# Optimization experiments

Measured on AMD Instinct MI355X. Metric: run time of the kernel, lower is better.

Reference implementation:

```python
import jax, jax.numpy as jnp
import numpy as np

H = 50000   # hidden_size
IN = 50000  # in_size
NNZ = 800000
B = 8
T = 32


def spmm(indices, values, num_rows, x):
    """COO sparse @ dense. indices: (2, nnz) int, values: (nnz,), x: (K, N)."""
    rows, cols = indices[0], indices[1]
    contrib = values[:, None] * x[cols]          # (nnz, N) gather + scale
    return jax.ops.segment_sum(contrib, rows, num_segments=num_rows)  # (M, N)


def setup_inputs() -> dict:
    key = jax.random.key(0)
    k1, k2, k3, k4, k5 = jax.random.split(key, 5)
    x = jax.random.normal(k1, (B, T, IN), dtype=jnp.float32)
    hh_indices = jax.random.randint(k2, (2, NNZ), 0, H)
    hh_values = jax.random.normal(k3, (NNZ,), dtype=jnp.float32) * 0.1
    hh_bias = jnp.zeros((H, 1), dtype=jnp.float32)
    ih_indices = jax.random.randint(k4, (2, NNZ), 0, IN)
    ih_values = jax.random.normal(k5, (NNZ,), dtype=jnp.float32) * 0.1
    return {"x": x, "hh_values": hh_values, "hh_bias": hh_bias,
            "ih_values": ih_values, "hh_indices": hh_indices,
            "ih_indices": ih_indices}


def reference(x, hh_values, hh_bias, ih_values, hh_indices, ih_indices):
    # x: (B, T, IN) batch_first -> (T, IN, B) as in _format_x
    xt = jnp.transpose(x, (1, 2, 0))
    h0 = jnp.zeros((H, x.shape[0]), dtype=x.dtype)  # zeros init, (H, B)

    def step(h, x_t):
        pre = (spmm(hh_indices, hh_values, H, h) + hh_bias
               + spmm(ih_indices, ih_values, H, x_t))
        h_new = jnp.tanh(pre)  # layernorm is Identity (use_layernorm=False)
        return h_new, h_new

    _, hs = jax.lax.scan(step, h0, xt)       # (T, H, B)
    return jnp.transpose(hs, (2, 0, 1))      # (B, T, H) batch_first
```

## Files before the change

### kernel.cpp

```cpp
#include <hip/hip_runtime.h>
#include <math.h>

#define HSZ 50000
#define INSZ 50000
#define NNZc 800000
#define BSZ 8
#define TSZ 32

#define CHUNK 2048
#define NBLK ((NNZc + CHUNK - 1) / CHUNK)
#define NCB 196
#define HWORDS (256 * NBLK)
#define NC2 ((HWORDS + 1023) / 1024)

#define NPB 1008
#define GRPS 8
#define GCNT (NPB / GRPS)
#define ROWS_SWEEP (NPB * 32)

typedef _Float16 half8 __attribute__((ext_vector_type(8)));
typedef _Float16 half4 __attribute__((ext_vector_type(4)));

__device__ __forceinline__ unsigned f2h_bits(float f) {
    _Float16 h = (_Float16)f;
    unsigned short u;
    __builtin_memcpy(&u, &h, 2);
    return (unsigned)u;
}
__device__ __forceinline__ float h_bits2f(unsigned u) {
    unsigned short us = (unsigned short)u;
    _Float16 h;
    __builtin_memcpy(&h, &us, 2);
    return (float)h;
}


__global__ void p1_count(const int* __restrict__ hh_idx, const int* __restrict__ ih_idx,
                         int* __restrict__ ghist) {
    const int* rows = blockIdx.y ? ih_idx : hh_idx;
    __shared__ int cnt[256];
    int tid = threadIdx.x;
    cnt[tid] = 0;
    __syncthreads();
    int base = blockIdx.x * CHUNK;
    int nElem = min(CHUNK, NNZc - base);
    for (int k = tid; k < nElem; k += 256) {
        atomicAdd(&cnt[rows[base + k] >> 8], 1);
    }
    __syncthreads();
    ghist[((size_t)blockIdx.y * 256 + tid) * NBLK + blockIdx.x] = cnt[tid];
}

__global__ void p2scanA(int* __restrict__ ghist, int* __restrict__ partials) {
    int* g = ghist + (size_t)blockIdx.y * HWORDS;
    __shared__ int sm[1024];
    int tid = threadIdx.x;
    int idx = blockIdx.x * 1024 + tid;
    int v = (idx < HWORDS) ? g[idx] : 0;
    sm[tid] = v;
    __syncthreads();
    int x = v;
    for (int off = 1; off < 1024; off <<= 1) {
        int y = (tid >= off) ? sm[tid - off] : 0;
        __syncthreads();
        x += y;
        sm[tid] = x;
        __syncthreads();
    }
    if (idx < HWORDS) g[idx] = x - v;
    if (tid == 1023) partials[blockIdx.y * 128 + blockIdx.x] = x;
}

__global__ void p2scanB(int* __restrict__ partials) {
    __shared__ int sm[128];
    int tid = threadIdx.x;
    for (int m = 0; m < 2; ++m) {
        int v = (tid < NC2) ? partials[m * 128 + tid] : 0;
        sm[tid] = v;
        __syncthreads();
        int x = v;
        for (int off = 1; off < 128; off <<= 1) {
            int y = (tid >= off) ? sm[tid - off] : 0;
            __syncthreads();
            x += y;
            sm[tid] = x;
            __syncthreads();
        }
        if (tid < NC2) partials[m * 128 + tid] = x - v;
        __syncthreads();
    }
}

__global__ void p2scanC(int* __restrict__ ghist, const int* __restrict__ partials,
                        int* __restrict__ cbs) {
    int mat = blockIdx.y;
    int* g = ghist + (size_t)mat * HWORDS;
    int i = blockIdx.x * 256 + threadIdx.x;
    if (i < HWORDS) {
        int v = g[i] + partials[mat * 128 + (i >> 10)];
        g[i] = v;
        int b = i / NBLK;
        if (i - b * NBLK == 0 && b < NCB) cbs[mat * (NCB + 1) + b] = v;
    }
    if (i == 0) cbs[mat * (NCB + 1) + NCB] = NNZc;
}

__global__ void p2_part(const int* __restrict__ hh_idx, const float* __restrict__ hh_v,
                        const int* __restrict__ ih_idx, const float* __restrict__ ih_v,
                        const int* __restrict__ ghist,
                        uint2* __restrict__ tmp_hh, uint2* __restrict__ tmp_ih) {
    int mat = blockIdx.y;
    const int* idx = mat ? ih_idx : hh_idx;
    const float* val = mat ? ih_v : hh_v;
    uint2* tmp = mat ? tmp_ih : tmp_hh;
    const int* g = ghist + (size_t)mat * HWORDS;

    __shared__ int cnt[256];
    __shared__ int lstart[256];
    __shared__ int scanbuf[256];
    __shared__ int gbase[256];
    __shared__ uint2 stage[CHUNK];

    int tid = threadIdx.x;
    int base = blockIdx.x * CHUNK;
    int nElem = min(CHUNK, NNZc - base);

    cnt[tid] = 0;
    gbase[tid] = g[(size_t)tid * NBLK + blockIdx.x];
    __syncthreads();
    for (int k = tid; k < nElem; k += 256) {
        atomicAdd(&cnt[idx[base + k] >> 8], 1);
    }
    __syncthreads();
    int v = cnt[tid];
    scanbuf[tid] = v;
    __syncthreads();
    int x = v;
    for (int off = 1; off < 256; off <<= 1) {
        int y = (tid >= off) ? scanbuf[tid - off] : 0;
        __syncthreads();
        x += y;
        scanbuf[tid] = x;
        __syncthreads();
    }
    lstart[tid] = x - v;
    cnt[tid] = 0;
    __syncthreads();
    for (int k = tid; k < nElem; k += 256) {
        int r = idx[base + k];
        int c = idx[NNZc + base + k];
        int b = r >> 8;
        int rank = atomicAdd(&cnt[b], 1);
        stage[lstart[b] + rank] = make_uint2(((unsigned)r << 16) | (unsigned)c,
                                             __float_as_uint(val[base + k]));
    }
    __syncthreads();
    for (int k = tid; k < nElem; k += 256) {
        uint2 el = stage[k];
        int b = el.x >> 24;
        tmp[gbase[b] + (k - lstart[b])] = el;
    }
}

__global__ void p3_final(const int* __restrict__ cbs,
                         const uint2* __restrict__ tmp_hh, const uint2* __restrict__ tmp_ih,
                         int* __restrict__ ptr_hh, int* __restrict__ ptr_ih,
                         unsigned* __restrict__ cv_hh, unsigned* __restrict__ cv_ih) {
    int mat = blockIdx.y;
    const uint2* tmp = mat ? tmp_ih : tmp_hh;
    int* ptr = mat ? ptr_ih : ptr_hh;
    unsigned* cv = mat ? cv_ih : cv_hh;
    __shared__ int rcnt[256];
    __shared__ int rstart[256];
    __shared__ int scanbuf[256];
    int cb = blockIdx.x;
    int row0 = cb << 8;
    int nrows = min(256, HSZ - row0);
    int s = cbs[mat * (NCB + 1) + cb];
    int e = cbs[mat * (NCB + 1) + cb + 1];
    int tid = threadIdx.x;
    rcnt[tid] = 0;
    __syncthreads();
    for (int k = s + tid; k < e; k += 256) {
        atomicAdd(&rcnt[(tmp[k].x >> 16) & 255], 1);
    }
    __syncthreads();
    int v = rcnt[tid];
    scanbuf[tid] = v;
    __syncthreads();
    int x = v;
    for (int off = 1; off < 256; off <<= 1) {
        int y = (tid >= off) ? scanbuf[tid - off] : 0;
        __syncthreads();
        x += y;
        scanbuf[tid] = x;
        __syncthreads();
    }
    rstart[tid] = x - v;
    if (tid < nrows) ptr[row0 + tid] = s + x - v;
    if (cb == NCB - 1 && tid == 0) ptr[HSZ] = NNZc;
    rcnt[tid] = 0;
    __syncthreads();
    for (int k = s + tid; k < e; k += 256) {
        uint2 el = tmp[k];
        int lr = (el.x >> 16) & 255;
        int rank = atomicAdd(&rcnt[lr], 1);
        cv[s + rstart[lr] + rank] =
            (f2h_bits(__uint_as_float(el.y)) << 16) | (el.x & 0xffffu);
    }
}


__global__ void transpose_x2(const float* __restrict__ x, _Float16* __restrict__ X2h) {
    extern __shared__ float tile[];
    int i0 = blockIdx.x * 64;
    int tid = threadIdx.x;
    int il = tid & 15;
    int tr = (tid >> 4) & 3;
    int tg = tid >> 6;
#pragma unroll
    for (int iter = 0; iter < 16; ++iter) {
        int tb = iter * 16 + tg * 4 + tr;
        int t = tb >> 3, b = tb & 7;
        const float4 v = *reinterpret_cast<const float4*>(
            x + ((size_t)b * TSZ + t) * INSZ + i0 + il * 4);
        tile[(il * 4 + 0) * 257 + tb] = v.x;
        tile[(il * 4 + 1) * 257 + tb] = v.y;
        tile[(il * 4 + 2) * 257 + tb] = v.z;
        tile[(il * 4 + 3) * 257 + tb] = v.w;
    }
    __syncthreads();
    for (int k = 0; k < 64; ++k) {
        int i = i0 + k;
        if (i < INSZ) X2h[(size_t)i * 256 + tid] = (_Float16)tile[k * 257 + tid];
    }
}


__global__ void ihc_kernel(const int* __restrict__ ptr, const unsigned* __restrict__ cv,
                           const float* __restrict__ bias, const half4* __restrict__ X2h,
                           half4* __restrict__ ihcT) {
    __shared__ half4 lds[4 * 65];
    int wid = threadIdx.x >> 6;
    int lane = threadIdx.x & 63;
    int r = (blockIdx.x << 2) + wid;
    int s = ptr[r], e = ptr[r + 1];
    s = __builtin_amdgcn_readfirstlane(s);
    e = __builtin_amdgcn_readfirstlane(e);
    float4 acc = make_float4(0.f, 0.f, 0.f, 0.f);
    int j = s;
    for (; j + 3 < e; j += 4) {
        unsigned a = cv[j], b = cv[j + 1], c = cv[j + 2], d = cv[j + 3];
        float va = h_bits2f(a >> 16);
        float vb = h_bits2f(b >> 16);
        float vc = h_bits2f(c >> 16);
        float vd = h_bits2f(d >> 16);
        half4 x0 = X2h[((size_t)(a & 0xffffu) << 6) + lane];
        half4 x1 = X2h[((size_t)(b & 0xffffu) << 6) + lane];
        half4 x2 = X2h[((size_t)(c & 0xffffu) << 6) + lane];
        half4 x3 = X2h[((size_t)(d & 0xffffu) << 6) + lane];
        acc.x = fmaf(va, (float)x0[0], acc.x);
        acc.y = fmaf(va, (float)x0[1], acc.y);
        acc.z = fmaf(va, (float)x0[2], acc.z);
        acc.w = fmaf(va, (float)x0[3], acc.w);
        acc.x = fmaf(vb, (float)x1[0], acc.x);
        acc.y = fmaf(vb, (float)x1[1], acc.y);
        acc.z = fmaf(vb, (float)x1[2], acc.z);
        acc.w = fmaf(vb, (float)x1[3], acc.w);
        acc.x = fmaf(vc, (float)x2[0], acc.x);
        acc.y = fmaf(vc, (float)x2[1], acc.y);
        acc.z = fmaf(vc, (float)x2[2], acc.z);
        acc.w = fmaf(vc, (float)x2[3], acc.w);
        acc.x = fmaf(vd, (float)x3[0], acc.x);
        acc.y = fmaf(vd, (float)x3[1], acc.y);
        acc.z = fmaf(vd, (float)x3[2], acc.z);
        acc.w = fmaf(vd, (float)x3[3], acc.w);
    }
    for (; j < e; ++j) {
        unsigned a = cv[j];
        float va = h_bits2f(a >> 16);
        half4 x0 = X2h[((size_t)(a & 0xffffu) << 6) + lane];
        acc.x = fmaf(va, (float)x0[0], acc.x);
        acc.y = fmaf(va, (float)x0[1], acc.y);
        acc.z = fmaf(va, (float)x0[2], acc.z);
        acc.w = fmaf(va, (float)x0[3], acc.w);
    }
    float bb = bias[r];
    half4 o;
    o[0] = (_Float16)(acc.x + bb);
    o[1] = (_Float16)(acc.y + bb);
    o[2] = (_Float16)(acc.z + bb);
    o[3] = (_Float16)(acc.w + bb);
    lds[wid * 65 + lane] = o;
    __syncthreads();
    int plane = threadIdx.x >> 3;
    int w = threadIdx.x & 7;
    int row = w >> 1, q = w & 1;
    int r2 = (blockIdx.x << 2) + row;
    ihcT[((size_t)plane * HSZ + r2) * 2 + q] = lds[row * 65 + 2 * plane + q];
}


__device__ __forceinline__ float fast_tanh(float x) {
    float e = __expf(2.0f * x);
    return 1.0f - __fdividef(2.0f, e + 1.0f);
}

__device__ __forceinline__ void grid_bar(int* __restrict__ ctl, int t) {
    __syncthreads();
    if (threadIdx.x == 0) {
        int g = blockIdx.x & 7;
        __hip_atomic_fetch_add(&ctl[g * 64 + t], 1, __ATOMIC_RELAXED,
                               __HIP_MEMORY_SCOPE_AGENT);
        if (blockIdx.x < 8) {
            while (__hip_atomic_load(&ctl[g * 64 + t], __ATOMIC_RELAXED,
                                     __HIP_MEMORY_SCOPE_AGENT) < GCNT)
                __builtin_amdgcn_s_sleep(1);
            __hip_atomic_fetch_add(&ctl[512 + t], 1, __ATOMIC_RELAXED,
                                   __HIP_MEMORY_SCOPE_AGENT);
            while (__hip_atomic_load(&ctl[512 + t], __ATOMIC_RELAXED,
                                     __HIP_MEMORY_SCOPE_AGENT) < GRPS)
                __builtin_amdgcn_s_sleep(1);
            __hip_atomic_store(&ctl[576 + g * 64], t + 1, __ATOMIC_RELAXED,
                               __HIP_MEMORY_SCOPE_AGENT);
        } else {
            while (__hip_atomic_load(&ctl[576 + g * 64], __ATOMIC_RELAXED,
                                     __HIP_MEMORY_SCOPE_AGENT) <= t)
                __builtin_amdgcn_s_sleep(8);
        }
    }
    __syncthreads();
}

__device__ __forceinline__ void do_row(int r, int s, int e, int t, int sub,
                                       const unsigned* __restrict__ cv,
                                       const half8* __restrict__ hprev,
                                       const half8* __restrict__ ihcT,
                                       unsigned long long* __restrict__ hw,
                                       float* __restrict__ out) {
    float a0 = 0.f, a1 = 0.f, a2 = 0.f, a3 = 0.f;
    float a4 = 0.f, a5 = 0.f, a6 = 0.f, a7 = 0.f;
    if (t > 0) {
        for (int j = s; j < e; j += 8) {
            unsigned u = cv[j];
            float v = h_bits2f(u >> 16);
            half8 hv = hprev[u & 0xffffu];
            a0 = fmaf(v, (float)hv[0], a0);
            a1 = fmaf(v, (float)hv[1], a1);
            a2 = fmaf(v, (float)hv[2], a2);
            a3 = fmaf(v, (float)hv[3], a3);
            a4 = fmaf(v, (float)hv[4], a4);
            a5 = fmaf(v, (float)hv[5], a5);
            a6 = fmaf(v, (float)hv[6], a6);
            a7 = fmaf(v, (float)hv[7], a7);
        }
    }
    a0 += __shfl_xor(a0, 1); a1 += __shfl_xor(a1, 1);
    a2 += __shfl_xor(a2, 1); a3 += __shfl_xor(a3, 1);
    a4 += __shfl_xor(a4, 1); a5 += __shfl_xor(a5, 1);
    a6 += __shfl_xor(a6, 1); a7 += __shfl_xor(a7, 1);
    a0 += __shfl_xor(a0, 2); a1 += __shfl_xor(a1, 2);
    a2 += __shfl_xor(a2, 2); a3 += __shfl_xor(a3, 2);
    a4 += __shfl_xor(a4, 2); a5 += __shfl_xor(a5, 2);
    a6 += __shfl_xor(a6, 2); a7 += __shfl_xor(a7, 2);
    a0 += __shfl_xor(a0, 4); a1 += __shfl_xor(a1, 4);
    a2 += __shfl_xor(a2, 4); a3 += __shfl_xor(a3, 4);
    a4 += __shfl_xor(a4, 4); a5 += __shfl_xor(a5, 4);
    a6 += __shfl_xor(a6, 4); a7 += __shfl_xor(a7, 4);
    if (sub == 0) {
        half8 b8 = ihcT[(size_t)t * HSZ + r];
        float h0 = fast_tanh(a0 + (float)b8[0]);
        float h1 = fast_tanh(a1 + (float)b8[1]);
        float h2 = fast_tanh(a2 + (float)b8[2]);
        float h3 = fast_tanh(a3 + (float)b8[3]);
        float h4 = fast_tanh(a4 + (float)b8[4]);
        float h5 = fast_tanh(a5 + (float)b8[5]);
        float h6 = fast_tanh(a6 + (float)b8[6]);
        float h7 = fast_tanh(a7 + (float)b8[7]);
        half8 hh;
        hh[0] = (_Float16)h0; hh[1] = (_Float16)h1;
        hh[2] = (_Float16)h2; hh[3] = (_Float16)h3;
        hh[4] = (_Float16)h4; hh[5] = (_Float16)h5;
        hh[6] = (_Float16)h6; hh[7] = (_Float16)h7;
        union { half8 h; unsigned long long q[2]; } u2;
        u2.h = hh;
        __hip_atomic_store(hw + ((size_t)r << 1), u2.q[0], __ATOMIC_RELAXED,
                           __HIP_MEMORY_SCOPE_AGENT);
        __hip_atomic_store(hw + ((size_t)r << 1) + 1, u2.q[1], __ATOMIC_RELAXED,
                           __HIP_MEMORY_SCOPE_AGENT);
        __builtin_nontemporal_store(h0, &out[((size_t)0 * TSZ + t) * HSZ + r]);
        __builtin_nontemporal_store(h1, &out[((size_t)1 * TSZ + t) * HSZ + r]);
        __builtin_nontemporal_store(h2, &out[((size_t)2 * TSZ + t) * HSZ + r]);
        __builtin_nontemporal_store(h3, &out[((size_t)3 * TSZ + t) * HSZ + r]);
        __builtin_nontemporal_store(h4, &out[((size_t)4 * TSZ + t) * HSZ + r]);
        __builtin_nontemporal_store(h5, &out[((size_t)5 * TSZ + t) * HSZ + r]);
        __builtin_nontemporal_store(h6, &out[((size_t)6 * TSZ + t) * HSZ + r]);
        __builtin_nontemporal_store(h7, &out[((size_t)7 * TSZ + t) * HSZ + r]);
    }
}

__global__ void __launch_bounds__(256, 4) steps_persist(
        const int* __restrict__ ptr, const unsigned* __restrict__ cv,
        const half8* __restrict__ ihcT, half8* __restrict__ hs,
        float* __restrict__ out, int* __restrict__ ctl) {
    int tid = threadIdx.x;
    int sub = tid & 7;
    int r0 = blockIdx.x * 32 + (tid >> 3);
    int r1 = r0 + ROWS_SWEEP;
    int s0 = ptr[r0] + sub, e0 = ptr[r0 + 1];
    bool has1 = (r1 < HSZ);
    int s1 = 0, e1 = 0;
    if (has1) { s1 = ptr[r1] + sub; e1 = ptr[r1 + 1]; }

    for (int t = 0; t < TSZ; ++t) {
        const half8* __restrict__ hprev = hs + (size_t)(t > 0 ? t - 1 : 0) * HSZ;
        unsigned long long* __restrict__ hw =
            (unsigned long long*)(hs + (size_t)t * HSZ);
        do_row(r0, s0, e0, t, sub, cv, hprev, ihcT, hw, out);
        if (has1) do_row(r1, s1, e1, t, sub, cv, hprev, ihcT, hw, out);
        if (t < TSZ - 1) grid_bar(ctl, t);
    }
}


static inline size_t align256(size_t x) { return (x + 255) & ~(size_t)255; }

extern "C" void kernel_launch(void* const* d_in, const int* in_sizes, int n_in,
                              void* d_out, int out_size, void* d_ws, size_t ws_size,
                              hipStream_t stream) {
    const float* x          = (const float*)d_in[0];
    const float* hh_values  = (const float*)d_in[1];
    const float* hh_bias    = (const float*)d_in[2];
    const float* ih_values  = (const float*)d_in[3];
    const int*   hh_indices = (const int*)d_in[4];
    const int*   ih_indices = (const int*)d_in[5];
    float* out = (float*)d_out;

    char* ws = (char*)d_ws;
    _Float16* X2h   = (_Float16*)ws; ws += align256((size_t)INSZ * 256 * 2);
    half8*  hs      = (half8*)X2h;
    half4*  ihcT    = (half4*)ws;  ws += align256((size_t)HSZ * 256 * 2);
    int*    hh_ptr  = (int*)ws;    ws += align256((size_t)(HSZ + 1) * 4);
    int*    ih_ptr  = (int*)ws;    ws += align256((size_t)(HSZ + 1) * 4);
    int*    ghist   = (int*)ws;    ws += align256((size_t)2 * HWORDS * 4);
    int*    partials= (int*)ws;    ws += align256((size_t)256 * 4);
    int*    cbs     = (int*)ws;    ws += align256((size_t)2 * (NCB + 1) * 4);
    int*    ctl     = (int*)ws;    ws += align256((size_t)1088 * 4);
    uint2*  tmp_hh  = (uint2*)ws;  ws += align256((size_t)NNZc * 8);
    uint2*  tmp_ih  = (uint2*)ws;  ws += align256((size_t)NNZc * 8);
    unsigned* cv_hh = (unsigned*)ws; ws += align256((size_t)NNZc * 4);
    unsigned* cv_ih = (unsigned*)ws; ws += align256((size_t)NNZc * 4);

    hipMemsetAsync(ctl, 0, (size_t)1088 * 4, stream);

    p1_count<<<dim3(NBLK, 2), 256, 0, stream>>>(hh_indices, ih_indices, ghist);
    p2scanA<<<dim3(NC2, 2), 1024, 0, stream>>>(ghist, partials);
    p2scanB<<<1, 128, 0, stream>>>(partials);
    p2scanC<<<dim3((HWORDS + 255) / 256, 2), 256, 0, stream>>>(ghist, partials, cbs);
    p2_part<<<dim3(NBLK, 2), 256, 0, stream>>>(hh_indices, hh_values, ih_indices, ih_values,
                                               ghist, tmp_hh, tmp_ih);
    p3_final<<<dim3(NCB, 2), 256, 0, stream>>>(cbs, tmp_hh, tmp_ih,
                                               hh_ptr, ih_ptr, cv_hh, cv_ih);

    transpose_x2<<<(INSZ + 63) / 64, 256, 64 * 257 * 4, stream>>>(x, X2h);
    ihc_kernel<<<HSZ / 4, 256, 0, stream>>>(ih_ptr, cv_ih, hh_bias, (const half4*)X2h, ihcT);

    steps_persist<<<NPB, 256, 0, stream>>>(hh_ptr, cv_hh, (const half8*)ihcT,
                                           hs, out, ctl);
}
```

Baseline: 553.1 us.

## Remap rows to 4-lane groups and add per-XCD prefetch of previous hidden state

Switches from 8 lanes per row with two row sweeps to 4 lanes per row, 64 rows per block, with 784 persistent blocks. Each lane now handles two nonzeros per iteration for more memory-level parallelism. Each group of 8 blocks also cooperatively loads a slice of the previous hidden state, intended to warm a per-XCD L2 cache before the gather. This trades more blocks doing redundant prefetch traffic for fewer gather stalls, and changes the shuffle reduction depth and block count, which also changes the grid barrier's group size.

```diff
diff --git a/kernel.cpp b/kernel.cpp
--- a/kernel.cpp
+++ b/kernel.cpp
@@ -13,10 +13,11 @@
 #define HWORDS (256 * NBLK)
 #define NC2 ((HWORDS + 1023) / 1024)
 
-#define NPB 1008
+#define NPB 784
 #define GRPS 8
 #define GCNT (NPB / GRPS)
-#define ROWS_SWEEP (NPB * 32)
+#define PFS (NPB / 8)
+#define PFPER ((HSZ * 2 + PFS - 1) / PFS)
 
 typedef _Float16 half8 __attribute__((ext_vector_type(8)));
 typedef _Float16 half4 __attribute__((ext_vector_type(4)));
@@ -332,92 +333,115 @@
     __syncthreads();
 }
 
-__device__ __forceinline__ void do_row(int r, int s, int e, int t, int sub,
-                                       const unsigned* __restrict__ cv,
-                                       const half8* __restrict__ hprev,
-                                       const half8* __restrict__ ihcT,
-                                       unsigned long long* __restrict__ hw,
-                                       float* __restrict__ out) {
-    float a0 = 0.f, a1 = 0.f, a2 = 0.f, a3 = 0.f;
-    float a4 = 0.f, a5 = 0.f, a6 = 0.f, a7 = 0.f;
-    if (t > 0) {
-        for (int j = s; j < e; j += 8) {
-            unsigned u = cv[j];
-            float v = h_bits2f(u >> 16);
-            half8 hv = hprev[u & 0xffffu];
-            a0 = fmaf(v, (float)hv[0], a0);
-            a1 = fmaf(v, (float)hv[1], a1);
-            a2 = fmaf(v, (float)hv[2], a2);
-            a3 = fmaf(v, (float)hv[3], a3);
-            a4 = fmaf(v, (float)hv[4], a4);
-            a5 = fmaf(v, (float)hv[5], a5);
-            a6 = fmaf(v, (float)hv[6], a6);
-            a7 = fmaf(v, (float)hv[7], a7);
-        }
-    }
-    a0 += __shfl_xor(a0, 1); a1 += __shfl_xor(a1, 1);
-    a2 += __shfl_xor(a2, 1); a3 += __shfl_xor(a3, 1);
-    a4 += __shfl_xor(a4, 1); a5 += __shfl_xor(a5, 1);
-    a6 += __shfl_xor(a6, 1); a7 += __shfl_xor(a7, 1);
-    a0 += __shfl_xor(a0, 2); a1 += __shfl_xor(a1, 2);
-    a2 += __shfl_xor(a2, 2); a3 += __shfl_xor(a3, 2);
-    a4 += __shfl_xor(a4, 2); a5 += __shfl_xor(a5, 2);
-    a6 += __shfl_xor(a6, 2); a7 += __shfl_xor(a7, 2);
-    a0 += __shfl_xor(a0, 4); a1 += __shfl_xor(a1, 4);
-    a2 += __shfl_xor(a2, 4); a3 += __shfl_xor(a3, 4);
-    a4 += __shfl_xor(a4, 4); a5 += __shfl_xor(a5, 4);
-    a6 += __shfl_xor(a6, 4); a7 += __shfl_xor(a7, 4);
-    if (sub == 0) {
-        half8 b8 = ihcT[(size_t)t * HSZ + r];
-        float h0 = fast_tanh(a0 + (float)b8[0]);
-        float h1 = fast_tanh(a1 + (float)b8[1]);
-        float h2 = fast_tanh(a2 + (float)b8[2]);
-        float h3 = fast_tanh(a3 + (float)b8[3]);
-        float h4 = fast_tanh(a4 + (float)b8[4]);
-        float h5 = fast_tanh(a5 + (float)b8[5]);
-        float h6 = fast_tanh(a6 + (float)b8[6]);
-        float h7 = fast_tanh(a7 + (float)b8[7]);
-        half8 hh;
-        hh[0] = (_Float16)h0; hh[1] = (_Float16)h1;
-        hh[2] = (_Float16)h2; hh[3] = (_Float16)h3;
-        hh[4] = (_Float16)h4; hh[5] = (_Float16)h5;
-        hh[6] = (_Float16)h6; hh[7] = (_Float16)h7;
-        union { half8 h; unsigned long long q[2]; } u2;
-        u2.h = hh;
-        __hip_atomic_store(hw + ((size_t)r << 1), u2.q[0], __ATOMIC_RELAXED,
-                           __HIP_MEMORY_SCOPE_AGENT);
-        __hip_atomic_store(hw + ((size_t)r << 1) + 1, u2.q[1], __ATOMIC_RELAXED,
-                           __HIP_MEMORY_SCOPE_AGENT);
-        __builtin_nontemporal_store(h0, &out[((size_t)0 * TSZ + t) * HSZ + r]);
-        __builtin_nontemporal_store(h1, &out[((size_t)1 * TSZ + t) * HSZ + r]);
-        __builtin_nontemporal_store(h2, &out[((size_t)2 * TSZ + t) * HSZ + r]);
-        __builtin_nontemporal_store(h3, &out[((size_t)3 * TSZ + t) * HSZ + r]);
-        __builtin_nontemporal_store(h4, &out[((size_t)4 * TSZ + t) * HSZ + r]);
-        __builtin_nontemporal_store(h5, &out[((size_t)5 * TSZ + t) * HSZ + r]);
-        __builtin_nontemporal_store(h6, &out[((size_t)6 * TSZ + t) * HSZ + r]);
-        __builtin_nontemporal_store(h7, &out[((size_t)7 * TSZ + t) * HSZ + r]);
-    }
-}
-
 __global__ void __launch_bounds__(256, 4) steps_persist(
         const int* __restrict__ ptr, const unsigned* __restrict__ cv,
         const half8* __restrict__ ihcT, half8* __restrict__ hs,
         float* __restrict__ out, int* __restrict__ ctl) {
     int tid = threadIdx.x;
-    int sub = tid & 7;
-    int r0 = blockIdx.x * 32 + (tid >> 3);
-    int r1 = r0 + ROWS_SWEEP;
-    int s0 = ptr[r0] + sub, e0 = ptr[r0 + 1];
-    bool has1 = (r1 < HSZ);
-    int s1 = 0, e1 = 0;
-    if (has1) { s1 = ptr[r1] + sub; e1 = ptr[r1 + 1]; }
+    int sub = tid & 3;
+    int r = blockIdx.x * 64 + (tid >> 2);
+    bool active = (r < HSZ);
+    int s = 0, e = 0;
+    if (active) { s = ptr[r]; e = ptr[r + 1]; }
+    int j0 = s + (sub << 1);
+    int pbase = (blockIdx.x >> 3) * PFPER + tid;
+    int pend = min((blockIdx.x >> 3) * PFPER + PFPER, HSZ * 2);
 
     for (int t = 0; t < TSZ; ++t) {
         const half8* __restrict__ hprev = hs + (size_t)(t > 0 ? t - 1 : 0) * HSZ;
         unsigned long long* __restrict__ hw =
             (unsigned long long*)(hs + (size_t)t * HSZ);
-        do_row(r0, s0, e0, t, sub, cv, hprev, ihcT, hw, out);
-        if (has1) do_row(r1, s1, e1, t, sub, cv, hprev, ihcT, hw, out);
+
+        float a0 = 0.f, a1 = 0.f, a2 = 0.f, a3 = 0.f;
+        float a4 = 0.f, a5 = 0.f, a6 = 0.f, a7 = 0.f;
+        if (t > 0) {
+            const unsigned long long* hp = (const unsigned long long*)hprev;
+            unsigned long long q0 = 0, q1 = 0, q2 = 0, q3 = 0;
+            if (pbase < pend)       q0 = hp[pbase];
+            if (pbase + 256 < pend) q1 = hp[pbase + 256];
+            if (pbase + 512 < pend) q2 = hp[pbase + 512];
+            if (pbase + 768 < pend) q3 = hp[pbase + 768];
+            if (active) {
+                int j = j0;
+                for (; j + 1 < e; j += 8) {
+                    unsigned u0 = cv[j];
+                    unsigned u1 = cv[j + 1];
+                    float v0 = h_bits2f(u0 >> 16);
+                    float v1 = h_bits2f(u1 >> 16);
+                    half8 hv0 = hprev[u0 & 0xffffu];
+                    half8 hv1 = hprev[u1 & 0xffffu];
+                    a0 = fmaf(v0, (float)hv0[0], a0);
+                    a1 = fmaf(v0, (float)hv0[1], a1);
+                    a2 = fmaf(v0, (float)hv0[2], a2);
+                    a3 = fmaf(v0, (float)hv0[3], a3);
+                    a4 = fmaf(v0, (float)hv0[4], a4);
+                    a5 = fmaf(v0, (float)hv0[5], a5);
+                    a6 = fmaf(v0, (float)hv0[6], a6);
+                    a7 = fmaf(v0, (float)hv0[7], a7);
+                    a0 = fmaf(v1, (float)hv1[0], a0);
+                    a1 = fmaf(v1, (float)hv1[1], a1);
+                    a2 = fmaf(v1, (float)hv1[2], a2);
+                    a3 = fmaf(v1, (float)hv1[3], a3);
+                    a4 = fmaf(v1, (float)hv1[4], a4);
+                    a5 = fmaf(v1, (float)hv1[5], a5);
+                    a6 = fmaf(v1, (float)hv1[6], a6);
+                    a7 = fmaf(v1, (float)hv1[7], a7);
+                }
+                if (j < e) {
+                    unsigned u0 = cv[j];
+                    float v0 = h_bits2f(u0 >> 16);
+                    half8 hv0 = hprev[u0 & 0xffffu];
+                    a0 = fmaf(v0, (float)hv0[0], a0);
+                    a1 = fmaf(v0, (float)hv0[1], a1);
+                    a2 = fmaf(v0, (float)hv0[2], a2);
+                    a3 = fmaf(v0, (float)hv0[3], a3);
+                    a4 = fmaf(v0, (float)hv0[4], a4);
+                    a5 = fmaf(v0, (float)hv0[5], a5);
+                    a6 = fmaf(v0, (float)hv0[6], a6);
+                    a7 = fmaf(v0, (float)hv0[7], a7);
+                }
+            }
+            asm volatile("" :: "v"(q0), "v"(q1), "v"(q2), "v"(q3));
+        }
+        a0 += __shfl_xor(a0, 1); a1 += __shfl_xor(a1, 1);
+        a2 += __shfl_xor(a2, 1); a3 += __shfl_xor(a3, 1);
+        a4 += __shfl_xor(a4, 1); a5 += __shfl_xor(a5, 1);
+        a6 += __shfl_xor(a6, 1); a7 += __shfl_xor(a7, 1);
+        a0 += __shfl_xor(a0, 2); a1 += __shfl_xor(a1, 2);
+        a2 += __shfl_xor(a2, 2); a3 += __shfl_xor(a3, 2);
+        a4 += __shfl_xor(a4, 2); a5 += __shfl_xor(a5, 2);
+        a6 += __shfl_xor(a6, 2); a7 += __shfl_xor(a7, 2);
+
+        if (active && sub == 0) {
+            half8 b8 = ihcT[(size_t)t * HSZ + r];
+            float h0 = fast_tanh(a0 + (float)b8[0]);
+            float h1 = fast_tanh(a1 + (float)b8[1]);
+            float h2 = fast_tanh(a2 + (float)b8[2]);
+            float h3 = fast_tanh(a3 + (float)b8[3]);
+            float h4 = fast_tanh(a4 + (float)b8[4]);
+            float h5 = fast_tanh(a5 + (float)b8[5]);
+            float h6 = fast_tanh(a6 + (float)b8[6]);
+            float h7 = fast_tanh(a7 + (float)b8[7]);
+            half8 hh;
+            hh[0] = (_Float16)h0; hh[1] = (_Float16)h1;
+            hh[2] = (_Float16)h2; hh[3] = (_Float16)h3;
+            hh[4] = (_Float16)h4; hh[5] = (_Float16)h5;
+            hh[6] = (_Float16)h6; hh[7] = (_Float16)h7;
+            union { half8 h; unsigned long long q[2]; } u2;
+            u2.h = hh;
+            __hip_atomic_store(hw + ((size_t)r << 1), u2.q[0], __ATOMIC_RELAXED,
+                               __HIP_MEMORY_SCOPE_AGENT);
+            __hip_atomic_store(hw + ((size_t)r << 1) + 1, u2.q[1], __ATOMIC_RELAXED,
+                               __HIP_MEMORY_SCOPE_AGENT);
+            __builtin_nontemporal_store(h0, &out[((size_t)0 * TSZ + t) * HSZ + r]);
+            __builtin_nontemporal_store(h1, &out[((size_t)1 * TSZ + t) * HSZ + r]);
+            __builtin_nontemporal_store(h2, &out[((size_t)2 * TSZ + t) * HSZ + r]);
+            __builtin_nontemporal_store(h3, &out[((size_t)3 * TSZ + t) * HSZ + r]);
+            __builtin_nontemporal_store(h4, &out[((size_t)4 * TSZ + t) * HSZ + r]);
+            __builtin_nontemporal_store(h5, &out[((size_t)5 * TSZ + t) * HSZ + r]);
+            __builtin_nontemporal_store(h6, &out[((size_t)6 * TSZ + t) * HSZ + r]);
+            __builtin_nontemporal_store(h7, &out[((size_t)7 * TSZ + t) * HSZ + r]);
+        }
         if (t < TSZ - 1) grid_bar(ctl, t);
     }
 }
```

After: 539.6 us. 2.4% less time.
